# Kernel tuning notes

Measured on AMD Instinct MI355X. Metric: run time of the kernel, lower is better.

The kernel has to match this reference:

```python
import jax, jax.numpy as jnp
import numpy as np

# Dimensions: D must equal C_CHUNK**2 (original code's view+transpose requires it)
D = 4096        # flattened input dim per sample
C_CHUNK = 64    # chunk_size (rows of G per chunk)
N_CHUNKS = D // C_CHUNK  # = 64
H = 512         # hidden dim of forward_func MLP
C_OUT = 8       # output classes of forward_func
B = 8           # batch size (state_batch has 2*B rows)
EPS_G = 1e-4    # metric regularizer (constant under grad)


def setup_inputs() -> dict:
    key = jax.random.key(0)
    ks = jax.random.split(key, 6)
    t = jax.random.uniform(ks[0], (1,), dtype=jnp.float32)
    state_batch = jax.random.normal(ks[1], (2 * B, D), dtype=jnp.float32)
    x0_batch = jax.random.normal(ks[2], (B, D), dtype=jnp.float32)
    x1_batch = jax.random.normal(ks[3], (B, D), dtype=jnp.float32)
    W1 = jax.random.normal(ks[4], (D, H), dtype=jnp.float32) / np.float32(np.sqrt(D))
    W2 = jax.random.normal(ks[5], (H, C_OUT), dtype=jnp.float32) / np.float32(np.sqrt(H))
    return {"t": t, "state_batch": state_batch, "x0_batch": x0_batch,
            "x1_batch": x1_batch, "W1": W1, "W2": W2}


def _accel_per_sample(x, v, W1, W2):
    """Chunked Christoffel-symbol contraction for one sample.
    x: [D] current point, v: [D] deviation velocity. Returns a: [D]."""
    def f(xi):  # forward_func: 2-layer tanh MLP, [D] -> [C_OUT]
        return jnp.tanh(xi @ W1) @ W2

    ones = jnp.ones((D,), x.dtype)

    def chunk_sums(xi):
        # G = J^T J + eps*I; row_sums[i] = sum_j G[i,j] computed without
        # materializing the D x D metric: J^T (J @ 1)  (+ const eps on diag).
        J = jax.jacrev(f)(xi)              # [C_OUT, D]
        row = J.T @ (J @ ones)             # [D]
        return row.reshape(N_CHUNKS, C_CHUNK).sum(axis=1)  # [N_CHUNKS]

    g = jax.jacrev(chunk_sums)(x)          # [N_CHUNKS, D] = dG_chunk_sum/dx
    g = g.reshape(N_CHUNKS, C_CHUNK, C_CHUNK)
    g = g / (jnp.linalg.norm(g, axis=2, keepdims=True) + 1e-6)
    Gamma = 0.5 * (g + jnp.swapaxes(g, 1, 2))   # symmetrized [nc, c, c]
    vc = v.reshape(N_CHUNKS, C_CHUNK)
    # a_chunk[i] = -sum_k Gamma[i,k] v_i v_k  (Christoffel quadratic in v)
    a = -jnp.einsum('nik,ni,nk->ni', Gamma, vc, vc)
    return a.reshape(D)


def reference(t, state_batch, x0_batch, x1_batch, W1, W2):
    ts = t[0]
    Bn = state_batch.shape[0] // 2
    deviation = state_batch[:Bn]
    dev_velocity = state_batch[Bn:]
    window = 4.0 * ts * (1.0 - ts)
    x = x0_batch + ts * (x1_batch - x0_batch) + window * deviation  # [B, D]
    a = jax.vmap(_accel_per_sample, in_axes=(0, 0, None, None))(x, dev_velocity, W1, W2)
    a = a / (jnp.linalg.norm(dev_velocity, axis=1, keepdims=True) + 1e-6)
    restoration = -0.1 * deviation
    return jnp.concatenate([dev_velocity, a + restoration], axis=0)  # [2B, D]
```

## Files before the change

kernel.cpp:

```cpp
#include <hip/hip_runtime.h>

#define D 4096
#define H 512
#define NCH 64
#define CCH 64
#define B 8
#define COUT 8

typedef __bf16 bf16x8 __attribute__((ext_vector_type(8)));
typedef float  f32x4  __attribute__((ext_vector_type(4)));

#define OFF_P    0
#define OFF_PHN  (OFF_P + NCH*H)
#define OFF_UPT  (OFF_PHN + H*NCH)
#define OFF_S    (OFF_UPT + B*H*NCH)
#define OFF_ST2  (OFF_S + B*H)
#define OFF_Q    (OFF_ST2 + B*H)
#define OFF_C    (OFF_Q + B*H)
#define OFF_VN   (OFF_C + H)
#define OFF_A1   (OFF_VN + 64)
#define OFF_ZB   (OFF_A1 + B*NCH*CCH)
#define OFF_W1H  (OFF_ZB + B*64*4096)
#define OFF_W1L  (OFF_W1H + (D*H)/2)
#define OFF_WH   (OFF_W1L + (D*H)/2)
#define OFF_WL   (OFF_WH + (B*NCH*H)/2)

__device__ __forceinline__ unsigned short f2bf(float x) {
    unsigned int u = __float_as_uint(x);
    unsigned int r = (u + 0x7FFFu + ((u >> 16) & 1u)) >> 16;
    return (unsigned short)r;
}
__device__ __forceinline__ float bf2f(unsigned short s) {
    return __uint_as_float(((unsigned int)s) << 16);
}

__global__ __launch_bounds__(256) void k1_reduce_w1(const float* __restrict__ W1,
                                                    const float* __restrict__ state,
                                                    const float* __restrict__ x0,
                                                    const float* __restrict__ x1,
                                                    const float* __restrict__ tptr,
                                                    float* __restrict__ ws) {
    int n   = blockIdx.x;
    int ht  = blockIdx.y;
    int tid = threadIdx.x;
    int hq  = ht * 32 + (tid & 31);
    int jh  = tid >> 5;

    __shared__ float xs[B][64];
    __shared__ f32x4 red[8][32][9];

    float ts = tptr[0];
    float window = 4.f * ts * (1.f - ts);
    if (tid < 64) {
        int d = n * 64 + tid;
        for (int b = 0; b < B; ++b) {
            float a0 = x0[b * D + d];
            float a1v = x1[b * D + d];
            float dev = state[b * D + d];
            xs[b][tid] = a0 + ts * (a1v - a0) + window * dev;
        }
    }
    __syncthreads();

    unsigned short* __restrict__ W1Hp = (unsigned short*)(ws + OFF_W1H);
    unsigned short* __restrict__ W1Lp = (unsigned short*)(ws + OFF_W1L);

    f32x4 p4 = {0.f, 0.f, 0.f, 0.f};
    f32x4 up[B];
#pragma unroll
    for (int b = 0; b < B; ++b) up[b] = p4;

#pragma unroll
    for (int jj = 0; jj < 8; ++jj) {
        int j = jh * 8 + jj;
        int d = n * 64 + j;
        f32x4 w = ((const f32x4*)W1)[d * (H / 4) + hq];
        p4 += w;
#pragma unroll
        for (int b = 0; b < B; ++b) up[b] += w * xs[b][j];
        unsigned short h0 = f2bf(w.x), h1 = f2bf(w.y), h2 = f2bf(w.z), h3 = f2bf(w.w);
        ushort4 hv = {h0, h1, h2, h3};
        ushort4 lv = {f2bf(w.x - bf2f(h0)), f2bf(w.y - bf2f(h1)),
                      f2bf(w.z - bf2f(h2)), f2bf(w.w - bf2f(h3))};
        *(ushort4*)(W1Hp + d * H + hq * 4) = hv;
        *(ushort4*)(W1Lp + d * H + hq * 4) = lv;
    }

    int l = tid & 31;
    red[jh][l][0] = p4;
#pragma unroll
    for (int b = 0; b < B; ++b) red[jh][l][1 + b] = up[b];
    __syncthreads();

    if (jh == 0) {
        f32x4 pt = red[0][l][0];
        f32x4 ut[B];
#pragma unroll
        for (int b = 0; b < B; ++b) ut[b] = red[0][l][1 + b];
        for (int g = 1; g < 8; ++g) {
            pt += red[g][l][0];
#pragma unroll
            for (int b = 0; b < B; ++b) ut[b] += red[g][l][1 + b];
        }
        *(f32x4*)(ws + OFF_P + n * H + hq * 4) = pt;
#pragma unroll
        for (int e = 0; e < 4; ++e) ws[OFF_PHN + (hq * 4 + e) * NCH + n] = pt[e];
#pragma unroll
        for (int b = 0; b < B; ++b)
#pragma unroll
            for (int e = 0; e < 4; ++e)
                ws[OFF_UPT + (b * H + hq * 4 + e) * NCH + n] = ut[b][e];
    }
}

__global__ void k2_sample(const float* __restrict__ W2,
                          const float* __restrict__ state,
                          float* __restrict__ ws) {
    int b = blockIdx.x, tid = threadIdx.x;
    int wid = tid >> 6, lane = tid & 63;
    __shared__ float lm[8][8];
    __shared__ float ms[8];
    __shared__ float lv[8];

    int h = tid;
    f32x4 u4 = {0.f, 0.f, 0.f, 0.f}, c4 = u4;
    const f32x4* upp = (const f32x4*)(ws + OFF_UPT + (b * H + h) * NCH);
    const f32x4* pp  = (const f32x4*)(ws + OFF_PHN + h * NCH);
#pragma unroll
    for (int j = 0; j < 16; ++j) { u4 += upp[j]; c4 += pp[j]; }
    float u = u4.x + u4.y + u4.z + u4.w;
    float c = c4.x + c4.y + c4.z + c4.w;

    float tt  = tanhf(u);
    float s   = 1.f - tt * tt;
    float st2 = -2.f * tt * s;
    ws[OFF_S   + b * H + h] = s;
    ws[OFF_ST2 + b * H + h] = st2;
    ws[OFF_C   + h] = c;

    const float4* w2p = (const float4*)(W2 + h * 8);
    float4 w2a = w2p[0], w2b = w2p[1];
    float w2r[8] = {w2a.x, w2a.y, w2a.z, w2a.w, w2b.x, w2b.y, w2b.z, w2b.w};

    float cs = c * s;
    float pr[8];
#pragma unroll
    for (int o = 0; o < 8; ++o) pr[o] = cs * w2r[o];
#pragma unroll
    for (int mk = 1; mk < 64; mk <<= 1)
#pragma unroll
        for (int o = 0; o < 8; ++o) pr[o] += __shfl_xor(pr[o], mk);
    if (lane == 0)
#pragma unroll
        for (int o = 0; o < 8; ++o) lm[wid][o] = pr[o];

    float v2 = 0.f;
    const float* v = state + (size_t)(B + b) * D;
#pragma unroll
    for (int j = 0; j < D / H; ++j) { float vv = v[j * H + h]; v2 += vv * vv; }
#pragma unroll
    for (int mk = 1; mk < 64; mk <<= 1) v2 += __shfl_xor(v2, mk);
    if (lane == 0) lv[wid] = v2;
    __syncthreads();

    if (tid < 8) {
        float a = 0.f;
        for (int w = 0; w < 8; ++w) a += lm[w][tid];
        ms[tid] = a;
    }
    if (tid == 0) {
        float a = 0.f;
        for (int w = 0; w < 8; ++w) a += lv[w];
        ws[OFF_VN + b] = sqrtf(a) + 1e-6f;
    }
    __syncthreads();

    float q = 0.f;
#pragma unroll
    for (int o = 0; o < 8; ++o) q += w2r[o] * ms[o];
    ws[OFF_Q + b * H + h] = q;
}

__global__ void k3_w(const float* __restrict__ W2,
                     float* __restrict__ ws) {
    int n = blockIdx.x, b = blockIdx.y, lane = threadIdx.x;
    float M[8];
#pragma unroll
    for (int o = 0; o < 8; ++o) M[o] = 0.f;
    for (int j = 0; j < 8; ++j) {
        int h = j * 64 + lane;
        float ps = ws[OFF_P + n * H + h] * ws[OFF_S + b * H + h];
        const float4* wp = (const float4*)(W2 + h * 8);
        float4 wa = wp[0], wb = wp[1];
        M[0] += ps * wa.x; M[1] += ps * wa.y; M[2] += ps * wa.z; M[3] += ps * wa.w;
        M[4] += ps * wb.x; M[5] += ps * wb.y; M[6] += ps * wb.z; M[7] += ps * wb.w;
    }
#pragma unroll
    for (int mk = 1; mk < 64; mk <<= 1)
#pragma unroll
        for (int o = 0; o < 8; ++o) M[o] += __shfl_xor(M[o], mk);

    unsigned short* __restrict__ WHp = (unsigned short*)(ws + OFF_WH);
    unsigned short* __restrict__ WLp = (unsigned short*)(ws + OFF_WL);
    for (int j = 0; j < 8; ++j) {
        int h = j * 64 + lane;
        const float4* wp = (const float4*)(W2 + h * 8);
        float4 wa = wp[0], wb = wp[1];
        float r = wa.x*M[0] + wa.y*M[1] + wa.z*M[2] + wa.w*M[3]
                + wb.x*M[4] + wb.y*M[5] + wb.z*M[6] + wb.w*M[7];
        float P = ws[OFF_P + n * H + h];
        float wv = ws[OFF_ST2 + b * H + h] * (P * ws[OFF_Q + b * H + h] + ws[OFF_C + h] * r);
        unsigned short hi = f2bf(wv);
        WHp[(b * NCH + n) * H + h] = hi;
        WLp[(b * NCH + n) * H + h] = f2bf(wv - bf2f(hi));
    }
}

__global__ __launch_bounds__(256) void k4_mfma(const float* __restrict__ state,
                                               float* __restrict__ ws) {
    int i   = blockIdx.x;
    int b   = blockIdx.y;
    int tid = threadIdx.x;
    int wid = tid >> 6, lane = tid & 63;
    int r16 = lane & 15;
    int kgrp = (lane >> 4) * 8;

    __shared__ float gp[2][64][67];
    __shared__ float coefs[64];

    const unsigned short* __restrict__ W1Hp = (const unsigned short*)(ws + OFF_W1H);
    const unsigned short* __restrict__ W1Lp = (const unsigned short*)(ws + OFF_W1L);
    const unsigned short* __restrict__ WHp  = (const unsigned short*)(ws + OFF_WH);
    const unsigned short* __restrict__ WLp  = (const unsigned short*)(ws + OFF_WL);

    f32x4 acc[4][4];
    f32x4 z4 = {0.f, 0.f, 0.f, 0.f};
#pragma unroll
    for (int m = 0; m < 4; ++m)
#pragma unroll
        for (int c = 0; c < 4; ++c) acc[m][c] = z4;

    int kb = wid * 128 + kgrp;
#pragma unroll
    for (int ks = 0; ks < 4; ++ks) {
        int k = kb + ks * 32;
        bf16x8 ah[4], al[4], bh[4], bl[4];
#pragma unroll
        for (int m = 0; m < 4; ++m) {
            int off = (b * 64 + m * 16 + r16) * H + k;
            ah[m] = *(const bf16x8*)(WHp + off);
            al[m] = *(const bf16x8*)(WLp + off);
        }
#pragma unroll
        for (int c = 0; c < 4; ++c) {
            int off = (i * 64 + c * 16 + r16) * H + k;
            bh[c] = *(const bf16x8*)(W1Hp + off);
            bl[c] = *(const bf16x8*)(W1Lp + off);
        }
#pragma unroll
        for (int m = 0; m < 4; ++m)
#pragma unroll
            for (int c = 0; c < 4; ++c) {
                acc[m][c] = __builtin_amdgcn_mfma_f32_16x16x32_bf16(ah[m], bh[c], acc[m][c], 0, 0, 0);
                acc[m][c] = __builtin_amdgcn_mfma_f32_16x16x32_bf16(ah[m], bl[c], acc[m][c], 0, 0, 0);
                acc[m][c] = __builtin_amdgcn_mfma_f32_16x16x32_bf16(al[m], bh[c], acc[m][c], 0, 0, 0);
            }
    }

    int rowb = (lane >> 4) * 4;
    if (wid < 2) {
        float (*g)[67] = gp[wid];
#pragma unroll
        for (int m = 0; m < 4; ++m)
#pragma unroll
            for (int c = 0; c < 4; ++c)
#pragma unroll
                for (int e = 0; e < 4; ++e)
                    g[m * 16 + rowb + e][c * 16 + r16] = acc[m][c][e];
    }
    __syncthreads();
    if (wid >= 2) {
        float (*g)[67] = gp[wid - 2];
#pragma unroll
        for (int m = 0; m < 4; ++m)
#pragma unroll
            for (int c = 0; c < 4; ++c)
#pragma unroll
                for (int e = 0; e < 4; ++e)
                    g[m * 16 + rowb + e][c * 16 + r16] += acc[m][c][e];
    }
    __syncthreads();

    const float* v = state + (size_t)(B + b) * D;

    if (tid < 64) {
        int n = tid;
        float ss = 0.f, y = 0.f;
#pragma unroll 8
        for (int k = 0; k < 64; ++k) {
            float g = gp[0][n][k] + gp[1][n][k];
            ss += g * g;
            y  += g * v[n * 64 + k];
        }
        float nrm = sqrtf(ss) + 1e-6f;
        ws[OFF_A1 + (size_t)(b * NCH + n) * CCH + i] = y / nrm;
        coefs[n] = v[n * 64 + i] / nrm;
    }
    __syncthreads();

    float* zb = ws + OFF_ZB + ((size_t)b * 64 + i) * 4096;
#pragma unroll
    for (int r = 0; r < 16; ++r) {
        int idx = tid + r * 256;
        int n = idx >> 6, k = idx & 63;
        zb[idx] = (gp[0][n][k] + gp[1][n][k]) * coefs[n];
    }
}

__global__ void k5_final(const float* __restrict__ state,
                         const float* __restrict__ ws,
                         float* __restrict__ out) {
    int idx = blockIdx.x * 256 + threadIdx.x;
    float vel = state[32768 + idx];
    out[idx] = vel;
    int b = idx >> 12, e = idx & 4095;
    const float* zb = ws + OFF_ZB + (size_t)b * 64 * 4096 + e;
    float z = 0.f;
#pragma unroll 8
    for (int i = 0; i < 64; ++i) z += zb[(size_t)i * 4096];
    float a1 = ws[OFF_A1 + (size_t)b * 4096 + e];
    float av = -0.5f * vel * (a1 + z) / ws[OFF_VN + b];
    out[32768 + idx] = av - 0.1f * state[idx];
}

extern "C" void kernel_launch(void* const* d_in, const int* in_sizes, int n_in,
                              void* d_out, int out_size, void* d_ws, size_t ws_size,
                              hipStream_t stream) {
    const float* t   = (const float*)d_in[0];
    const float* st  = (const float*)d_in[1];
    const float* x0  = (const float*)d_in[2];
    const float* x1  = (const float*)d_in[3];
    const float* W1  = (const float*)d_in[4];
    const float* W2  = (const float*)d_in[5];
    float* out = (float*)d_out;
    float* ws  = (float*)d_ws;

    hipLaunchKernelGGL(k1_reduce_w1, dim3(64, 4), dim3(256), 0, stream, W1, st, x0, x1, t, ws);
    hipLaunchKernelGGL(k2_sample,    dim3(8),     dim3(512), 0, stream, W2, st, ws);
    hipLaunchKernelGGL(k3_w,         dim3(64, 8), dim3(64),  0, stream, W2, ws);
    hipLaunchKernelGGL(k4_mfma,      dim3(64, 8), dim3(256), 0, stream, st, ws);
    hipLaunchKernelGGL(k5_final,     dim3(128),   dim3(256), 0, stream, st, ws, out);
}
```

Baseline: 121.8 us.

## Fuse k2/k3 into one kernel, double-buffer k4 loads, pack two tiles per block

Merges the per-sample tanh kernel with the W-construction kernel, keeping s, st2, c and q in shared memory so global round-trips and one launch go away. The fused kernel now runs on only 8 blocks, so the W construction (previously 512 blocks) becomes much more serial. k4 now processes two (i,b) tiles per 512-thread block with register double-buffered bf16 fragment loads, meant to overlap memory latency with the MFMAs. k5 switches to 512-thread blocks.

New measurement: 153.0 us. 25.7% more time.

```diff
diff --git a/kernel.cpp b/kernel.cpp
--- a/kernel.cpp
+++ b/kernel.cpp
@@ -5,7 +5,6 @@
 #define NCH 64
 #define CCH 64
 #define B 8
-#define COUT 8
 
 typedef __bf16 bf16x8 __attribute__((ext_vector_type(8)));
 typedef float  f32x4  __attribute__((ext_vector_type(4)));
@@ -13,11 +12,7 @@
 #define OFF_P    0
 #define OFF_PHN  (OFF_P + NCH*H)
 #define OFF_UPT  (OFF_PHN + H*NCH)
-#define OFF_S    (OFF_UPT + B*H*NCH)
-#define OFF_ST2  (OFF_S + B*H)
-#define OFF_Q    (OFF_ST2 + B*H)
-#define OFF_C    (OFF_Q + B*H)
-#define OFF_VN   (OFF_C + H)
+#define OFF_VN   (OFF_UPT + B*H*NCH)
 #define OFF_A1   (OFF_VN + 64)
 #define OFF_ZB   (OFF_A1 + B*NCH*CCH)
 #define OFF_W1H  (OFF_ZB + B*64*4096)
@@ -113,11 +108,13 @@
     }
 }
 
-__global__ void k2_sample(const float* __restrict__ W2,
-                          const float* __restrict__ state,
-                          float* __restrict__ ws) {
+__global__ __launch_bounds__(512) void k23(const float* __restrict__ W2,
+                                           const float* __restrict__ state,
+                                           float* __restrict__ ws) {
     int b = blockIdx.x, tid = threadIdx.x;
     int wid = tid >> 6, lane = tid & 63;
+
+    __shared__ float sS[512], sS2[512], sC[512], sQ[512];
     __shared__ float lm[8][8];
     __shared__ float ms[8];
     __shared__ float lv[8];
@@ -134,9 +131,7 @@
     float tt  = tanhf(u);
     float s   = 1.f - tt * tt;
     float st2 = -2.f * tt * s;
-    ws[OFF_S   + b * H + h] = s;
-    ws[OFF_ST2 + b * H + h] = st2;
-    ws[OFF_C   + h] = c;
+    sS[h] = s; sS2[h] = st2; sC[h] = c;
 
     const float4* w2p = (const float4*)(W2 + h * 8);
     float4 w2a = w2p[0], w2b = w2p[1];
@@ -178,55 +173,62 @@
     float q = 0.f;
 #pragma unroll
     for (int o = 0; o < 8; ++o) q += w2r[o] * ms[o];
-    ws[OFF_Q + b * H + h] = q;
-}
-
-__global__ void k3_w(const float* __restrict__ W2,
-                     float* __restrict__ ws) {
-    int n = blockIdx.x, b = blockIdx.y, lane = threadIdx.x;
-    float M[8];
-#pragma unroll
-    for (int o = 0; o < 8; ++o) M[o] = 0.f;
-    for (int j = 0; j < 8; ++j) {
-        int h = j * 64 + lane;
-        float ps = ws[OFF_P + n * H + h] * ws[OFF_S + b * H + h];
-        const float4* wp = (const float4*)(W2 + h * 8);
-        float4 wa = wp[0], wb = wp[1];
-        M[0] += ps * wa.x; M[1] += ps * wa.y; M[2] += ps * wa.z; M[3] += ps * wa.w;
-        M[4] += ps * wb.x; M[5] += ps * wb.y; M[6] += ps * wb.z; M[7] += ps * wb.w;
-    }
-#pragma unroll
-    for (int mk = 1; mk < 64; mk <<= 1)
-#pragma unroll
-        for (int o = 0; o < 8; ++o) M[o] += __shfl_xor(M[o], mk);
+    sQ[h] = q;
+    __syncthreads();
 
     unsigned short* __restrict__ WHp = (unsigned short*)(ws + OFF_WH);
     unsigned short* __restrict__ WLp = (unsigned short*)(ws + OFF_WL);
-    for (int j = 0; j < 8; ++j) {
-        int h = j * 64 + lane;
-        const float4* wp = (const float4*)(W2 + h * 8);
-        float4 wa = wp[0], wb = wp[1];
-        float r = wa.x*M[0] + wa.y*M[1] + wa.z*M[2] + wa.w*M[3]
-                + wb.x*M[4] + wb.y*M[5] + wb.z*M[6] + wb.w*M[7];
-        float P = ws[OFF_P + n * H + h];
-        float wv = ws[OFF_ST2 + b * H + h] * (P * ws[OFF_Q + b * H + h] + ws[OFF_C + h] * r);
-        unsigned short hi = f2bf(wv);
-        WHp[(b * NCH + n) * H + h] = hi;
-        WLp[(b * NCH + n) * H + h] = f2bf(wv - bf2f(hi));
-    }
-}
-
-__global__ __launch_bounds__(256) void k4_mfma(const float* __restrict__ state,
-                                               float* __restrict__ ws) {
-    int i   = blockIdx.x;
-    int b   = blockIdx.y;
-    int tid = threadIdx.x;
-    int wid = tid >> 6, lane = tid & 63;
-    int r16 = lane & 15;
+
+    for (int it = 0; it < 8; ++it) {
+        int n = it * 8 + wid;
+        float M[8];
+#pragma unroll
+        for (int o = 0; o < 8; ++o) M[o] = 0.f;
+#pragma unroll
+        for (int j = 0; j < 8; ++j) {
+            int hh = j * 64 + lane;
+            float ps = ws[OFF_P + n * H + hh] * sS[hh];
+            const float4* wp = (const float4*)(W2 + hh * 8);
+            float4 wa = wp[0], wb = wp[1];
+            M[0] += ps * wa.x; M[1] += ps * wa.y; M[2] += ps * wa.z; M[3] += ps * wa.w;
+            M[4] += ps * wb.x; M[5] += ps * wb.y; M[6] += ps * wb.z; M[7] += ps * wb.w;
+        }
+#pragma unroll
+        for (int mk = 1; mk < 64; mk <<= 1)
+#pragma unroll
+            for (int o = 0; o < 8; ++o) M[o] += __shfl_xor(M[o], mk);
+
+#pragma unroll
+        for (int j = 0; j < 8; ++j) {
+            int hh = j * 64 + lane;
+            const float4* wp = (const float4*)(W2 + hh * 8);
+            float4 wa = wp[0], wb = wp[1];
+            float r = wa.x*M[0] + wa.y*M[1] + wa.z*M[2] + wa.w*M[3]
+                    + wb.x*M[4] + wb.y*M[5] + wb.z*M[6] + wb.w*M[7];
+            float P = ws[OFF_P + n * H + hh];
+            float wval = sS2[hh] * (P * sQ[hh] + sC[hh] * r);
+            unsigned short hi = f2bf(wval);
+            WHp[(b * NCH + n) * H + hh] = hi;
+            WLp[(b * NCH + n) * H + hh] = f2bf(wval - bf2f(hi));
+        }
+    }
+}
+
+__global__ __launch_bounds__(512, 2) void k4_mfma(const float* __restrict__ state,
+                                                  float* __restrict__ ws) {
+    int bid  = blockIdx.x;
+    int tid  = threadIdx.x;
+    int g    = tid >> 8;
+    int gt   = tid & 255;
+    int u    = bid * 2 + g;
+    int i    = u >> 3, b = u & 7;
+    int wvid = gt >> 6;
+    int lane = tid & 63;
+    int r16  = lane & 15;
     int kgrp = (lane >> 4) * 8;
 
-    __shared__ float gp[2][64][67];
-    __shared__ float coefs[64];
+    __shared__ float gp[2][2][64][67];
+    __shared__ float coefs[2][64];
 
     const unsigned short* __restrict__ W1Hp = (const unsigned short*)(ws + OFF_W1H);
     const unsigned short* __restrict__ W1Lp = (const unsigned short*)(ws + OFF_W1L);
@@ -234,93 +236,105 @@
     const unsigned short* __restrict__ WLp  = (const unsigned short*)(ws + OFF_WL);
 
     f32x4 acc[4][4];
-    f32x4 z4 = {0.f, 0.f, 0.f, 0.f};
+    f32x4 zz = {0.f, 0.f, 0.f, 0.f};
 #pragma unroll
     for (int m = 0; m < 4; ++m)
 #pragma unroll
-        for (int c = 0; c < 4; ++c) acc[m][c] = z4;
-
-    int kb = wid * 128 + kgrp;
-#pragma unroll
-    for (int ks = 0; ks < 4; ++ks) {
-        int k = kb + ks * 32;
-        bf16x8 ah[4], al[4], bh[4], bl[4];
-#pragma unroll
-        for (int m = 0; m < 4; ++m) {
-            int off = (b * 64 + m * 16 + r16) * H + k;
-            ah[m] = *(const bf16x8*)(WHp + off);
-            al[m] = *(const bf16x8*)(WLp + off);
-        }
-#pragma unroll
-        for (int c = 0; c < 4; ++c) {
-            int off = (i * 64 + c * 16 + r16) * H + k;
-            bh[c] = *(const bf16x8*)(W1Hp + off);
-            bl[c] = *(const bf16x8*)(W1Lp + off);
-        }
+        for (int c = 0; c < 4; ++c) acc[m][c] = zz;
+
+    int kb    = wvid * 128 + kgrp;
+    int baseA = (b * 64 + r16) * H;
+    int baseB = (i * 64 + r16) * H;
+
+    bf16x8 A0[8], B0[8], A1[8], B1[8];
+
+#define LOADF(FA, FB, KOFS) do {                                           \
+        int k_ = (KOFS);                                                   \
+        _Pragma("unroll")                                                  \
+        for (int m_ = 0; m_ < 4; ++m_) {                                   \
+            int oA = baseA + m_ * 16 * H + k_;                             \
+            FA[m_]     = *(const bf16x8*)(WHp + oA);                       \
+            FA[4 + m_] = *(const bf16x8*)(WLp + oA);                       \
+            int oB = baseB + m_ * 16 * H + k_;                             \
+            FB[m_]     = *(const bf16x8*)(W1Hp + oB);                      \
+            FB[4 + m_] = *(const bf16x8*)(W1Lp + oB);                      \
+        } } while (0)
+
+#define MFMA12(FA, FB) do {                                                \
+        _Pragma("unroll")                                                  \
+        for (int m = 0; m < 4; ++m)                                        \
+        _Pragma("unroll")                                                  \
+        for (int c = 0; c < 4; ++c) {                                      \
+            acc[m][c] = __builtin_amdgcn_mfma_f32_16x16x32_bf16(FA[m], FB[c], acc[m][c], 0, 0, 0);       \
+            acc[m][c] = __builtin_amdgcn_mfma_f32_16x16x32_bf16(FA[m], FB[4 + c], acc[m][c], 0, 0, 0);   \
+            acc[m][c] = __builtin_amdgcn_mfma_f32_16x16x32_bf16(FA[4 + m], FB[c], acc[m][c], 0, 0, 0);   \
+        } } while (0)
+
+    LOADF(A0, B0, kb);
+    LOADF(A1, B1, kb + 32);
+    MFMA12(A0, B0);
+    LOADF(A0, B0, kb + 64);
+    MFMA12(A1, B1);
+    LOADF(A1, B1, kb + 96);
+    MFMA12(A0, B0);
+    MFMA12(A1, B1);
+
+#undef LOADF
+#undef MFMA12
+
+    int rowb = (lane >> 4) * 4;
+    if (wvid < 2) {
+        float (*gpp)[67] = gp[g][wvid];
 #pragma unroll
         for (int m = 0; m < 4; ++m)
 #pragma unroll
-            for (int c = 0; c < 4; ++c) {
-                acc[m][c] = __builtin_amdgcn_mfma_f32_16x16x32_bf16(ah[m], bh[c], acc[m][c], 0, 0, 0);
-                acc[m][c] = __builtin_amdgcn_mfma_f32_16x16x32_bf16(ah[m], bl[c], acc[m][c], 0, 0, 0);
-                acc[m][c] = __builtin_amdgcn_mfma_f32_16x16x32_bf16(al[m], bh[c], acc[m][c], 0, 0, 0);
-            }
-    }
-
-    int rowb = (lane >> 4) * 4;
-    if (wid < 2) {
-        float (*g)[67] = gp[wid];
+            for (int c = 0; c < 4; ++c)
+#pragma unroll
+                for (int e = 0; e < 4; ++e)
+                    gpp[m * 16 + rowb + e][c * 16 + r16] = acc[m][c][e];
+    }
+    __syncthreads();
+    if (wvid >= 2) {
+        float (*gpp)[67] = gp[g][wvid - 2];
 #pragma unroll
         for (int m = 0; m < 4; ++m)
 #pragma unroll
             for (int c = 0; c < 4; ++c)
 #pragma unroll
                 for (int e = 0; e < 4; ++e)
-                    g[m * 16 + rowb + e][c * 16 + r16] = acc[m][c][e];
-    }
-    __syncthreads();
-    if (wid >= 2) {
-        float (*g)[67] = gp[wid - 2];
-#pragma unroll
-        for (int m = 0; m < 4; ++m)
-#pragma unroll
-            for (int c = 0; c < 4; ++c)
-#pragma unroll
-                for (int e = 0; e < 4; ++e)
-                    g[m * 16 + rowb + e][c * 16 + r16] += acc[m][c][e];
+                    gpp[m * 16 + rowb + e][c * 16 + r16] += acc[m][c][e];
     }
     __syncthreads();
 
     const float* v = state + (size_t)(B + b) * D;
-
-    if (tid < 64) {
-        int n = tid;
+    if (gt < 64) {
+        int n = gt;
         float ss = 0.f, y = 0.f;
 #pragma unroll 8
         for (int k = 0; k < 64; ++k) {
-            float g = gp[0][n][k] + gp[1][n][k];
-            ss += g * g;
-            y  += g * v[n * 64 + k];
+            float gv = gp[g][0][n][k] + gp[g][1][n][k];
+            ss += gv * gv;
+            y  += gv * v[n * 64 + k];
         }
         float nrm = sqrtf(ss) + 1e-6f;
         ws[OFF_A1 + (size_t)(b * NCH + n) * CCH + i] = y / nrm;
-        coefs[n] = v[n * 64 + i] / nrm;
+        coefs[g][n] = v[n * 64 + i] / nrm;
     }
     __syncthreads();
 
     float* zb = ws + OFF_ZB + ((size_t)b * 64 + i) * 4096;
 #pragma unroll
     for (int r = 0; r < 16; ++r) {
-        int idx = tid + r * 256;
+        int idx = gt + r * 256;
         int n = idx >> 6, k = idx & 63;
-        zb[idx] = (gp[0][n][k] + gp[1][n][k]) * coefs[n];
+        zb[idx] = (gp[g][0][n][k] + gp[g][1][n][k]) * coefs[g][n];
     }
 }
 
 __global__ void k5_final(const float* __restrict__ state,
                          const float* __restrict__ ws,
                          float* __restrict__ out) {
-    int idx = blockIdx.x * 256 + threadIdx.x;
+    int idx = blockIdx.x * 512 + threadIdx.x;
     float vel = state[32768 + idx];
     out[idx] = vel;
     int b = idx >> 12, e = idx & 4095;
@@ -346,8 +360,7 @@
     float* ws  = (float*)d_ws;
 
     hipLaunchKernelGGL(k1_reduce_w1, dim3(64, 4), dim3(256), 0, stream, W1, st, x0, x1, t, ws);
-    hipLaunchKernelGGL(k2_sample,    dim3(8),     dim3(512), 0, stream, W2, st, ws);
-    hipLaunchKernelGGL(k3_w,         dim3(64, 8), dim3(64),  0, stream, W2, ws);
-    hipLaunchKernelGGL(k4_mfma,      dim3(64, 8), dim3(256), 0, stream, st, ws);
-    hipLaunchKernelGGL(k5_final,     dim3(128),   dim3(256), 0, stream, st, ws, out);
-}
+    hipLaunchKernelGGL(k23,          dim3(8),     dim3(512), 0, stream, W2, st, ws);
+    hipLaunchKernelGGL(k4_mfma,      dim3(256),   dim3(512), 0, stream, st, ws);
+    hipLaunchKernelGGL(k5_final,     dim3(64),    dim3(512), 0, stream, st, ws, out);
+}
```
